# Kernel tuning notes

Hardware: AMD Instinct MI355X
Metric: run time of the kernel (lower is better)

Reference implementation:

```python
import jax, jax.numpy as jnp
import numpy as np

ALPHA = 0.2  # LeakyReLU negative slope
NEG_INF = -9e15


def setup_inputs() -> dict:
    key = jax.random.key(0)
    k1, k2, k3, k4, k5 = jax.random.split(key, 5)
    B, N, D = 4, 4096, 256
    feat = jax.random.normal(k1, (B, N, D), dtype=jnp.float32)
    adj = jax.random.randint(k2, (B, N, N), 0, 2, dtype=jnp.int32)
    W = jax.random.normal(k3, (D, D), dtype=jnp.float32) * (1.414 / np.sqrt(D))
    a_1 = jax.random.normal(k4, (D, 1), dtype=jnp.float32) * 0.1
    a_2 = jax.random.normal(k5, (D, 1), dtype=jnp.float32) * 0.1
    return {"feat": feat, "adj": adj, "W": W, "a_1": a_1, "a_2": a_2}


def reference(feat, adj, W, a_1, a_2):
    # h: [B, N, D]
    h = jnp.matmul(feat, W)
    Ax = jnp.matmul(h, a_1)  # [B, N, 1]
    Ay = jnp.matmul(h, a_2)  # [B, N, 1]
    # logits[b, i, j] = Ax[b, j] + Ay[b, i]
    logits = jnp.swapaxes(Ax, 1, 2) + Ay  # [B, N, N]
    e = jax.nn.leaky_relu(logits, negative_slope=ALPHA)
    e = jnp.where(adj > 0, e, jnp.float32(NEG_INF))
    attention = jax.nn.softmax(e, axis=-1)  # dropout p=0.0 -> identity
    h_prime = jnp.matmul(attention, feat)  # [B, N, in_features]
    h_out = jnp.matmul(h_prime, W)  # [B, N, out_features]
    return jax.nn.elu(h_out)
```

## Files before the change

kernel.cpp:

```cpp
#include <hip/hip_runtime.h>

typedef __attribute__((ext_vector_type(8))) short short8;
typedef __attribute__((ext_vector_type(4))) float f32x4;
typedef __attribute__((ext_vector_type(4))) int i32x4;
typedef __attribute__((ext_vector_type(2))) unsigned u32x2;

#define LOG2E 1.44269504f

__device__ __forceinline__ short f2bf(float f) {
  unsigned u = __builtin_bit_cast(unsigned, f);
  u += 0x7fffu + ((u >> 16) & 1u);
  return (short)(u >> 16);
}

__global__ __launch_bounds__(256) void gat_pro(
    const float* __restrict__ feat, const float* __restrict__ W,
    const float* __restrict__ a1, const float* __restrict__ a2,
    short* __restrict__ featB, short* __restrict__ WB,
    float* __restrict__ AxL, float* __restrict__ AyL) {
  __shared__ __align__(16) float a1f[256], a2f[256];
  __shared__ __align__(16) float w1f[256], w2f[256];
  __shared__ __align__(16) float tile[32][260];
  const int tid = threadIdx.x;
  const int f = blockIdx.x, b = blockIdx.y;

  a1f[tid] = a1[tid];
  a2f[tid] = a2[tid];
  __syncthreads();

  {
    float s1 = 0.f, s2 = 0.f;
    const float4* wr = (const float4*)(W + (size_t)tid * 256);
    for (int d0 = 0; d0 < 64; ++d0) {
      float4 v = wr[d0];
      s1 += v.x * a1f[d0 * 4] + v.y * a1f[d0 * 4 + 1] + v.z * a1f[d0 * 4 + 2] + v.w * a1f[d0 * 4 + 3];
      s2 += v.x * a2f[d0 * 4] + v.y * a2f[d0 * 4 + 1] + v.z * a2f[d0 * 4 + 2] + v.w * a2f[d0 * 4 + 3];
    }
    w1f[tid] = s1;
    w2f[tid] = s2;
  }
  __syncthreads();

  {
    const int r = tid >> 3, g8 = tid & 7;
    const float* frow = feat + ((size_t)(b * 4096 + f * 32 + r)) * 256;
    float s1 = 0.f, s2 = 0.f;
#pragma unroll
    for (int k = 0; k < 8; ++k) {
      const int c4 = g8 + 8 * k;
      float4 v = *(const float4*)(frow + c4 * 4);
      float4 u1 = *(const float4*)&w1f[c4 * 4];
      float4 u2 = *(const float4*)&w2f[c4 * 4];
      s1 += v.x * u1.x + v.y * u1.y + v.z * u1.z + v.w * u1.w;
      s2 += v.x * u2.x + v.y * u2.y + v.z * u2.z + v.w * u2.w;
      *(float4*)&tile[r][c4 * 4] = v;
    }
#pragma unroll
    for (int off = 4; off >= 1; off >>= 1) {
      s1 += __shfl_xor(s1, off);
      s2 += __shfl_xor(s2, off);
    }
    if (g8 == 0) {
      AxL[b * 4096 + f * 32 + r] = s1 * LOG2E;
      AyL[b * 4096 + f * 32 + r] = s2 * LOG2E;
    }
  }
  __syncthreads();

  {
    const int g = tid >> 4, l15 = tid & 15;
    short* d = featB + (((size_t)((b * 128 + f) * 16 + g)) * 64) * 8;
#pragma unroll
    for (int q = 0; q < 4; ++q) {
      short8 v;
#pragma unroll
      for (int j8 = 0; j8 < 8; ++j8) v[j8] = f2bf(tile[q * 8 + j8][g * 16 + l15]);
      *(short8*)(d + (q * 16 + l15) * 8) = v;
    }
  }

  if (b == 0 && f < 8) {
    const int g = tid >> 4, l15 = tid & 15;
    const float* s = W + ((size_t)f * 32) * 256 + g * 16 + l15;
    short* d = WB + (((size_t)(f * 16 + g)) * 64) * 8;
#pragma unroll
    for (int q = 0; q < 4; ++q) {
      short8 v;
#pragma unroll
      for (int j8 = 0; j8 < 8; ++j8) v[j8] = f2bf(s[(q * 8 + j8) * 256]);
      *(short8*)(d + (q * 16 + l15) * 8) = v;
    }
  }
}

__global__ __launch_bounds__(512, 2) void gat_attn(
    const short* __restrict__ featB,
    const int* __restrict__ adj,
    const float* __restrict__ AxL, const float* __restrict__ AyL,
    const short* __restrict__ WB,
    float* __restrict__ out)
{
  __shared__ short smem[33792];
  __shared__ float mred[8];

  const int tid = threadIdx.x;
  const int blk = blockIdx.x;
  const int x = blk & 7;
  const int b = x >> 1;
  const int it = ((blk >> 3) << 1) | (x & 1);
  const int i0 = it << 6;
  const int scoff = (blk >> 3) & 15;

  const int lane = tid & 63;
  const int aw = tid >> 6;

  const float* axb = AxL + b * 4096;
  float mx = -3.4e38f;
  for (int i = tid; i < 4096; i += 512) mx = fmaxf(mx, axb[i]);
#pragma unroll
  for (int off = 32; off >= 1; off >>= 1) mx = fmaxf(mx, __shfl_xor(mx, off));
  if (lane == 0) mred[aw] = mx;
  __syncthreads();
  const float MbLb = fmaxf(fmaxf(fmaxf(mred[0], mred[1]), fmaxf(mred[2], mred[3])),
                           fmaxf(fmaxf(mred[4], mred[5]), fmaxf(mred[6], mred[7])));

  float aLk[8], ddk[8];
#pragma unroll
  for (int k = 0; k < 8; ++k) {
    float ayL = AyL[b * 4096 + i0 + aw * 8 + k];
    float sL = ayL + MbLb;
    float mrL = fmaxf(sL, 0.2f * sL);
    aLk[k] = ayL - mrL;
    ddk[k] = -0.8f * mrL;
  }
  const int* adjr = adj + ((size_t)(b * 4096 + i0 + aw * 8)) * 4096 + lane * 4;
  const float4* axp = (const float4*)(AxL + b * 4096) + lane;

  const int cg2 = aw << 1;
  const int l15 = lane & 15;
  const int q = lane >> 4;

  f32x4 acc[4][2], lac[4];
#pragma unroll
  for (int r = 0; r < 4; ++r) {
    lac[r] = (f32x4){0.f, 0.f, 0.f, 0.f};
#pragma unroll
    for (int j = 0; j < 2; ++j) acc[r][j] = (f32x4){0.f, 0.f, 0.f, 0.f};
  }

  short8 ones;
#pragma unroll
  for (int j = 0; j < 8; ++j) ones[j] = (short)0x3F80;

  const short* fbb = featB + (size_t)b * 128 * 16 * 64 * 8 + lane * 8;

  i32x4 adv[8];
  float4 axv;
  {
    const int w0 = scoff;
    axv = axp[w0 * 64];
#pragma unroll
    for (int k = 0; k < 8; ++k)
      adv[k] = __builtin_nontemporal_load((const i32x4*)(adjr) + (size_t)k * 1024 + w0 * 64);
  }

  for (int sc = 0; sc < 16; ++sc) {
    const int wsc = (scoff + sc) & 15;
    const int pb = (sc & 1) * 16896;
    {
      const float* af = (const float*)&axv;
#pragma unroll
      for (int k = 0; k < 8; ++k) {
        unsigned pr[4];
#pragma unroll
        for (int u = 0; u < 4; ++u) {
          float v = af[u] + aLk[k];
          float uu = fmaxf(v, fmaf(0.2f, v, ddk[k]));
          unsigned ub = adv[k][u] > 0 ? __builtin_bit_cast(unsigned, uu) : 0xFF800000u;
          float p = __builtin_amdgcn_exp2f(__builtin_bit_cast(float, ub));
          pr[u] = __builtin_bit_cast(unsigned, p) + 0x8000u;
        }
        u32x2 pw;
        pw[0] = __builtin_amdgcn_perm(pr[1], pr[0], 0x07060302u);
        pw[1] = __builtin_amdgcn_perm(pr[3], pr[2], 0x07060302u);
        *(u32x2*)(smem + pb + (aw * 8 + k) * 264 + lane * 4) = pw;
      }
    }
    __syncthreads();

    if (sc < 15) {
      const int wn = (scoff + sc + 1) & 15;
      axv = axp[wn * 64];
#pragma unroll
      for (int k = 0; k < 8; ++k)
        adv[k] = __builtin_nontemporal_load((const i32x4*)(adjr) + (size_t)k * 1024 + wn * 64);
    }

#pragma unroll
    for (int h = 0; h < 8; ++h) {
      const int f = wsc * 8 + h;
      const short* fb = fbb + (((size_t)f * 16 + cg2) << 9);
      short8 a[4];
#pragma unroll
      for (int r = 0; r < 4; ++r)
        a[r] = *(const short8*)(smem + pb + (r * 16 + l15) * 264 + h * 32 + q * 8);
#pragma unroll
      for (int r = 0; r < 4; ++r)
        lac[r] = __builtin_amdgcn_mfma_f32_16x16x32_bf16(a[r], ones, lac[r], 0, 0, 0);
#pragma unroll
      for (int ct = 0; ct < 2; ++ct) {
        short8 bf = *(const short8*)(fb + (ct << 9));
#pragma unroll
        for (int r = 0; r < 4; ++r)
          acc[r][ct] = __builtin_amdgcn_mfma_f32_16x16x32_bf16(a[r], bf, acc[r][ct], 0, 0, 0);
      }
    }
  }

  float linv[4][4];
#pragma unroll
  for (int r = 0; r < 4; ++r)
#pragma unroll
    for (int reg = 0; reg < 4; ++reg) {
      float l = lac[r][reg];
      linv[r][reg] = l > 0.f ? 1.f / l : 0.f;
    }

  __syncthreads();
  short* hbuf = smem;
#pragma unroll
  for (int r = 0; r < 4; ++r)
#pragma unroll
    for (int reg = 0; reg < 4; ++reg) {
      const int lr = r * 16 + q * 4 + reg;
#pragma unroll
      for (int ct = 0; ct < 2; ++ct)
        hbuf[lr * 264 + (cg2 + ct) * 16 + l15] = f2bf(acc[r][ct][reg] * linv[r][reg]);
    }
  __syncthreads();

  const int rowg = (aw & 1) << 4;
  const int cgrp = (aw >> 1) << 2;

  f32x4 ac2[2][4];
#pragma unroll
  for (int r = 0; r < 2; ++r)
#pragma unroll
    for (int j = 0; j < 4; ++j) ac2[r][j] = (f32x4){0.f, 0.f, 0.f, 0.f};

  const short* wbb = WB + lane * 8;
#pragma unroll
  for (int f = 0; f < 8; ++f) {
    short8 a0 = *(const short8*)&hbuf[(rowg + l15) * 264 + f * 32 + q * 8];
    short8 a1 = *(const short8*)&hbuf[(rowg + 32 + l15) * 264 + f * 32 + q * 8];
    const short* wb = wbb + (((size_t)f * 16 + cgrp) << 9);
#pragma unroll
    for (int ct = 0; ct < 4; ++ct) {
      short8 bf = *(const short8*)(wb + (ct << 9));
      ac2[0][ct] = __builtin_amdgcn_mfma_f32_16x16x32_bf16(a0, bf, ac2[0][ct], 0, 0, 0);
      ac2[1][ct] = __builtin_amdgcn_mfma_f32_16x16x32_bf16(a1, bf, ac2[1][ct], 0, 0, 0);
    }
  }

#pragma unroll
  for (int r = 0; r < 2; ++r)
#pragma unroll
    for (int reg = 0; reg < 4; ++reg) {
      const int row = i0 + rowg + r * 32 + q * 4 + reg;
      float* orow = out + ((size_t)(b * 4096 + row)) * 256 + cgrp * 16 + l15;
#pragma unroll
      for (int ct = 0; ct < 4; ++ct) {
        float v = ac2[r][ct][reg];
        float o = v > 0.f ? v : (__builtin_amdgcn_exp2f(v * LOG2E) - 1.f);
        __builtin_nontemporal_store(o, orow + ct * 16);
      }
    }
}

extern "C" void kernel_launch(void* const* d_in, const int* in_sizes, int n_in,
                              void* d_out, int out_size, void* d_ws, size_t ws_size,
                              hipStream_t stream) {
  (void)in_sizes; (void)n_in; (void)out_size; (void)ws_size;
  const float* feat = (const float*)d_in[0];
  const int* adj = (const int*)d_in[1];
  const float* W = (const float*)d_in[2];
  const float* a1 = (const float*)d_in[3];
  const float* a2 = (const float*)d_in[4];
  float* out = (float*)d_out;

  char* ws = (char*)d_ws;
  short* featB   = (short*)ws;
  short* WB      = (short*)(ws + 8388608);
  float* AxL     = (float*)(ws + 8519680);
  float* AyL     = (float*)(ws + 8585216);

  hipLaunchKernelGGL(gat_pro, dim3(128, 4), dim3(256), 0, stream, feat, W, a1, a2, featB, WB, AxL, AyL);
  hipLaunchKernelGGL(gat_attn, dim3(256), dim3(512), 0, stream, featB, adj, AxL, AyL, WB, out);
}
```

Baseline: 410.0 us.

## Prefetch adjacency two super-chunks ahead with ping-pong register buffers

Restructures the main loop into unrolled even/odd pairs, each with its own register buffer for adjacency and Ax values. The global loads for a chunk are now issued two iterations ahead instead of one, giving them more time to cover memory latency. __syncthreads is replaced by an explicit LDS waitcnt plus s_barrier, so the barrier no longer waits on outstanding global loads. The cost is a second set of prefetch registers, which may lower occupancy or cause spills.

```diff
diff --git a/kernel.cpp b/kernel.cpp
--- a/kernel.cpp
+++ b/kernel.cpp
@@ -154,48 +154,33 @@
 
   const short* fbb = featB + (size_t)b * 128 * 16 * 64 * 8 + lane * 8;
 
-  i32x4 adv[8];
-  float4 axv;
-  {
-    const int w0 = scoff;
-    axv = axp[w0 * 64];
-#pragma unroll
-    for (int k = 0; k < 8; ++k)
-      adv[k] = __builtin_nontemporal_load((const i32x4*)(adjr) + (size_t)k * 1024 + w0 * 64);
-  }
-
-  for (int sc = 0; sc < 16; ++sc) {
+  i32x4 advE[8], advO[8];
+  float4 axvE, axvO;
+
+  auto phase1 = [&](int sc, const i32x4 (&advU)[8], const float4& axvU) {
+    const int pb = (sc & 1) * 16896;
+    const float* af = (const float*)&axvU;
+#pragma unroll
+    for (int k = 0; k < 8; ++k) {
+      unsigned pr[4];
+#pragma unroll
+      for (int u = 0; u < 4; ++u) {
+        float v = af[u] + aLk[k];
+        float uu = fmaxf(v, fmaf(0.2f, v, ddk[k]));
+        unsigned ub = advU[k][u] > 0 ? __builtin_bit_cast(unsigned, uu) : 0xFF800000u;
+        float p = __builtin_amdgcn_exp2f(__builtin_bit_cast(float, ub));
+        pr[u] = __builtin_bit_cast(unsigned, p) + 0x8000u;
+      }
+      u32x2 pw;
+      pw[0] = __builtin_amdgcn_perm(pr[1], pr[0], 0x07060302u);
+      pw[1] = __builtin_amdgcn_perm(pr[3], pr[2], 0x07060302u);
+      *(u32x2*)(smem + pb + (aw * 8 + k) * 264 + lane * 4) = pw;
+    }
+  };
+
+  auto phase2 = [&](int sc) {
     const int wsc = (scoff + sc) & 15;
     const int pb = (sc & 1) * 16896;
-    {
-      const float* af = (const float*)&axv;
-#pragma unroll
-      for (int k = 0; k < 8; ++k) {
-        unsigned pr[4];
-#pragma unroll
-        for (int u = 0; u < 4; ++u) {
-          float v = af[u] + aLk[k];
-          float uu = fmaxf(v, fmaf(0.2f, v, ddk[k]));
-          unsigned ub = adv[k][u] > 0 ? __builtin_bit_cast(unsigned, uu) : 0xFF800000u;
-          float p = __builtin_amdgcn_exp2f(__builtin_bit_cast(float, ub));
-          pr[u] = __builtin_bit_cast(unsigned, p) + 0x8000u;
-        }
-        u32x2 pw;
-        pw[0] = __builtin_amdgcn_perm(pr[1], pr[0], 0x07060302u);
-        pw[1] = __builtin_amdgcn_perm(pr[3], pr[2], 0x07060302u);
-        *(u32x2*)(smem + pb + (aw * 8 + k) * 264 + lane * 4) = pw;
-      }
-    }
-    __syncthreads();
-
-    if (sc < 15) {
-      const int wn = (scoff + sc + 1) & 15;
-      axv = axp[wn * 64];
-#pragma unroll
-      for (int k = 0; k < 8; ++k)
-        adv[k] = __builtin_nontemporal_load((const i32x4*)(adjr) + (size_t)k * 1024 + wn * 64);
-    }
-
 #pragma unroll
     for (int h = 0; h < 8; ++h) {
       const int f = wsc * 8 + h;
@@ -214,6 +199,49 @@
         for (int r = 0; r < 4; ++r)
           acc[r][ct] = __builtin_amdgcn_mfma_f32_16x16x32_bf16(a[r], bf, acc[r][ct], 0, 0, 0);
       }
+    }
+  };
+
+  {
+    const int w0 = scoff, w1 = (scoff + 1) & 15;
+    axvE = axp[w0 * 64];
+#pragma unroll
+    for (int k = 0; k < 8; ++k)
+      advE[k] = __builtin_nontemporal_load((const i32x4*)(adjr) + (size_t)k * 1024 + w0 * 64);
+    axvO = axp[w1 * 64];
+#pragma unroll
+    for (int k = 0; k < 8; ++k)
+      advO[k] = __builtin_nontemporal_load((const i32x4*)(adjr) + (size_t)k * 1024 + w1 * 64);
+  }
+
+  for (int scp = 0; scp < 8; ++scp) {
+    {
+      const int sc = 2 * scp;
+      phase1(sc, advE, axvE);
+      asm volatile("s_waitcnt lgkmcnt(0)" ::: "memory");
+      __builtin_amdgcn_s_barrier();
+      if (sc < 14) {
+        const int wn = (scoff + sc + 2) & 15;
+        axvE = axp[wn * 64];
+#pragma unroll
+        for (int k = 0; k < 8; ++k)
+          advE[k] = __builtin_nontemporal_load((const i32x4*)(adjr) + (size_t)k * 1024 + wn * 64);
+      }
+      phase2(sc);
+    }
+    {
+      const int sc = 2 * scp + 1;
+      phase1(sc, advO, axvO);
+      asm volatile("s_waitcnt lgkmcnt(0)" ::: "memory");
+      __builtin_amdgcn_s_barrier();
+      if (sc < 14) {
+        const int wn = (scoff + sc + 2) & 15;
+        axvO = axp[wn * 64];
+#pragma unroll
+        for (int k = 0; k < 8; ++k)
+          advO[k] = __builtin_nontemporal_load((const i32x4*)(adjr) + (size_t)k * 1024 + wn * 64);
+      }
+      phase2(sc);
     }
   }
 
```

Measured after the change: 409.7 us. About the same (-0.1%).

## Double chunk width per pipeline stage with dynamic shared memory and fewer barriers

Applied to the files above, without the earlier changes.

The column chunk per pipeline step grows from 256 to 512 columns, so the loop runs 8 iterations instead of 16. Each iteration prefetches twice as many adjacency vectors, and the double-buffered probability tile moves to about 130KB of dynamic shared memory. The goal is to halve the number of block barriers and give each step more MFMA work to hide global loads behind. The costs are occupancy dropping to one block per CU (launch bounds 512,1) and more registers held for prefetched adjacency data.

```diff
diff --git a/kernel.cpp b/kernel.cpp
--- a/kernel.cpp
+++ b/kernel.cpp
@@ -93,14 +93,14 @@
   }
 }
 
-__global__ __launch_bounds__(512, 2) void gat_attn(
+extern "C" __global__ __launch_bounds__(512, 1) void gat_attn(
     const short* __restrict__ featB,
     const int* __restrict__ adj,
     const float* __restrict__ AxL, const float* __restrict__ AyL,
     const short* __restrict__ WB,
     float* __restrict__ out)
 {
-  __shared__ short smem[33792];
+  extern __shared__ short smem[];
   __shared__ float mred[8];
 
   const int tid = threadIdx.x;
@@ -109,7 +109,7 @@
   const int b = x >> 1;
   const int it = ((blk >> 3) << 1) | (x & 1);
   const int i0 = it << 6;
-  const int scoff = (blk >> 3) & 15;
+  const int scoff = (blk >> 3) & 7;
 
   const int lane = tid & 63;
   const int aw = tid >> 6;
@@ -154,56 +154,68 @@
 
   const short* fbb = featB + (size_t)b * 128 * 16 * 64 * 8 + lane * 8;
 
-  i32x4 adv[8];
-  float4 axv;
+  i32x4 adv[16];
+  float4 axv0, axv1;
+
   {
-    const int w0 = scoff;
-    axv = axp[w0 * 64];
-#pragma unroll
-    for (int k = 0; k < 8; ++k)
-      adv[k] = __builtin_nontemporal_load((const i32x4*)(adjr) + (size_t)k * 1024 + w0 * 64);
-  }
-
-  for (int sc = 0; sc < 16; ++sc) {
-    const int wsc = (scoff + sc) & 15;
-    const int pb = (sc & 1) * 16896;
+    const int w = scoff;
+    axv0 = axp[w * 128];
+    axv1 = axp[w * 128 + 64];
+#pragma unroll
+    for (int k = 0; k < 8; ++k) {
+      adv[k * 2 + 0] = __builtin_nontemporal_load((const i32x4*)(adjr) + (size_t)k * 1024 + w * 128);
+      adv[k * 2 + 1] = __builtin_nontemporal_load((const i32x4*)(adjr) + (size_t)k * 1024 + w * 128 + 64);
+    }
+  }
+
+  for (int sc = 0; sc < 8; ++sc) {
+    const int wsc = (scoff + sc) & 7;
+    const int pb = (sc & 1) * 33280;
     {
-      const float* af = (const float*)&axv;
 #pragma unroll
       for (int k = 0; k < 8; ++k) {
-        unsigned pr[4];
-#pragma unroll
-        for (int u = 0; u < 4; ++u) {
-          float v = af[u] + aLk[k];
-          float uu = fmaxf(v, fmaf(0.2f, v, ddk[k]));
-          unsigned ub = adv[k][u] > 0 ? __builtin_bit_cast(unsigned, uu) : 0xFF800000u;
-          float p = __builtin_amdgcn_exp2f(__builtin_bit_cast(float, ub));
-          pr[u] = __builtin_bit_cast(unsigned, p) + 0x8000u;
+#pragma unroll
+        for (int c = 0; c < 2; ++c) {
+          const float* af = (c == 0) ? (const float*)&axv0 : (const float*)&axv1;
+          const i32x4 ad = adv[k * 2 + c];
+          unsigned pr[4];
+#pragma unroll
+          for (int u = 0; u < 4; ++u) {
+            float v = af[u] + aLk[k];
+            float uu = fmaxf(v, fmaf(0.2f, v, ddk[k]));
+            unsigned ub = ad[u] > 0 ? __builtin_bit_cast(unsigned, uu) : 0xFF800000u;
+            float p = __builtin_amdgcn_exp2f(__builtin_bit_cast(float, ub));
+            pr[u] = __builtin_bit_cast(unsigned, p) + 0x8000u;
+          }
+          u32x2 pw;
+          pw[0] = __builtin_amdgcn_perm(pr[1], pr[0], 0x07060302u);
+          pw[1] = __builtin_amdgcn_perm(pr[3], pr[2], 0x07060302u);
+          *(u32x2*)(smem + pb + (aw * 8 + k) * 520 + c * 256 + lane * 4) = pw;
         }
-        u32x2 pw;
-        pw[0] = __builtin_amdgcn_perm(pr[1], pr[0], 0x07060302u);
-        pw[1] = __builtin_amdgcn_perm(pr[3], pr[2], 0x07060302u);
-        *(u32x2*)(smem + pb + (aw * 8 + k) * 264 + lane * 4) = pw;
       }
     }
-    __syncthreads();
-
-    if (sc < 15) {
-      const int wn = (scoff + sc + 1) & 15;
-      axv = axp[wn * 64];
-#pragma unroll
-      for (int k = 0; k < 8; ++k)
-        adv[k] = __builtin_nontemporal_load((const i32x4*)(adjr) + (size_t)k * 1024 + wn * 64);
-    }
-
-#pragma unroll
-    for (int h = 0; h < 8; ++h) {
-      const int f = wsc * 8 + h;
+    asm volatile("s_waitcnt lgkmcnt(0)" ::: "memory");
+    __builtin_amdgcn_s_barrier();
+
+    if (sc < 7) {
+      const int wn = (scoff + sc + 1) & 7;
+      axv0 = axp[wn * 128];
+      axv1 = axp[wn * 128 + 64];
+#pragma unroll
+      for (int k = 0; k < 8; ++k) {
+        adv[k * 2 + 0] = __builtin_nontemporal_load((const i32x4*)(adjr) + (size_t)k * 1024 + wn * 128);
+        adv[k * 2 + 1] = __builtin_nontemporal_load((const i32x4*)(adjr) + (size_t)k * 1024 + wn * 128 + 64);
+      }
+    }
+
+#pragma unroll
+    for (int h = 0; h < 16; ++h) {
+      const int f = wsc * 16 + h;
       const short* fb = fbb + (((size_t)f * 16 + cg2) << 9);
       short8 a[4];
 #pragma unroll
       for (int r = 0; r < 4; ++r)
-        a[r] = *(const short8*)(smem + pb + (r * 16 + l15) * 264 + h * 32 + q * 8);
+        a[r] = *(const short8*)(smem + pb + (r * 16 + l15) * 520 + h * 32 + q * 8);
 #pragma unroll
       for (int r = 0; r < 4; ++r)
         lac[r] = __builtin_amdgcn_mfma_f32_16x16x32_bf16(a[r], ones, lac[r], 0, 0, 0);
@@ -295,5 +307,5 @@
   float* AyL     = (float*)(ws + 8585216);
 
   hipLaunchKernelGGL(gat_pro, dim3(128, 4), dim3(256), 0, stream, feat, W, a1, a2, featB, WB, AxL, AyL);
-  hipLaunchKernelGGL(gat_attn, dim3(256), dim3(512), 0, stream, featB, adj, AxL, AyL, WB, out);
+  hipLaunchKernelGGL(gat_attn, dim3(256), dim3(512), 133120, stream, featB, adj, AxL, AyL, WB, out);
 }
```

New measurement: 423.5 us. 1.03x slower.

## Use 1024-thread blocks in attention kernel, halving per-wave rows and columns

Applied to the files above, without the earlier changes.

Doubles the attention kernel's block size to 16 waves. Each wave now handles 4 adjacency rows and one 16-column output group instead of 8 rows and two groups, so per-thread registers drop and more waves are resident to hide adjacency-load latency. The __syncthreads in the main loop becomes an explicit lgkmcnt wait plus s_barrier, which no longer waits for the in-flight prefetch loads. The risk is that the per-sc barrier now spans 16 waves, and launch_bounds(1024,4) may not be attainable with 66KB of shared memory per block, which could limit occupancy.

```diff
diff --git a/kernel.cpp b/kernel.cpp
--- a/kernel.cpp
+++ b/kernel.cpp
@@ -93,7 +93,7 @@
   }
 }
 
-__global__ __launch_bounds__(512, 2) void gat_attn(
+__global__ __launch_bounds__(1024, 4) void gat_attn(
     const short* __restrict__ featB,
     const int* __restrict__ adj,
     const float* __restrict__ AxL, const float* __restrict__ AyL,
@@ -101,7 +101,7 @@
     float* __restrict__ out)
 {
   __shared__ short smem[33792];
-  __shared__ float mred[8];
+  __shared__ float mred[16];
 
   const int tid = threadIdx.x;
   const int blk = blockIdx.x;
@@ -113,39 +113,37 @@
 
   const int lane = tid & 63;
   const int aw = tid >> 6;
+  const int l15 = lane & 15;
+  const int q = lane >> 4;
 
   const float* axb = AxL + b * 4096;
   float mx = -3.4e38f;
-  for (int i = tid; i < 4096; i += 512) mx = fmaxf(mx, axb[i]);
+  for (int i = tid; i < 4096; i += 1024) mx = fmaxf(mx, axb[i]);
 #pragma unroll
   for (int off = 32; off >= 1; off >>= 1) mx = fmaxf(mx, __shfl_xor(mx, off));
   if (lane == 0) mred[aw] = mx;
   __syncthreads();
-  const float MbLb = fmaxf(fmaxf(fmaxf(mred[0], mred[1]), fmaxf(mred[2], mred[3])),
-                           fmaxf(fmaxf(mred[4], mred[5]), fmaxf(mred[6], mred[7])));
-
-  float aLk[8], ddk[8];
-#pragma unroll
-  for (int k = 0; k < 8; ++k) {
-    float ayL = AyL[b * 4096 + i0 + aw * 8 + k];
+  float MbLb = mred[0];
+#pragma unroll
+  for (int i = 1; i < 16; ++i) MbLb = fmaxf(MbLb, mred[i]);
+
+  float aLk[4], ddk[4];
+#pragma unroll
+  for (int k = 0; k < 4; ++k) {
+    float ayL = AyL[b * 4096 + i0 + aw * 4 + k];
     float sL = ayL + MbLb;
     float mrL = fmaxf(sL, 0.2f * sL);
     aLk[k] = ayL - mrL;
     ddk[k] = -0.8f * mrL;
   }
-  const int* adjr = adj + ((size_t)(b * 4096 + i0 + aw * 8)) * 4096 + lane * 4;
+  const int* adjr = adj + ((size_t)(b * 4096 + i0 + aw * 4)) * 4096 + lane * 4;
   const float4* axp = (const float4*)(AxL + b * 4096) + lane;
 
-  const int cg2 = aw << 1;
-  const int l15 = lane & 15;
-  const int q = lane >> 4;
-
-  f32x4 acc[4][2], lac[4];
+  f32x4 acc[4], lac[4];
 #pragma unroll
   for (int r = 0; r < 4; ++r) {
     lac[r] = (f32x4){0.f, 0.f, 0.f, 0.f};
-#pragma unroll
-    for (int j = 0; j < 2; ++j) acc[r][j] = (f32x4){0.f, 0.f, 0.f, 0.f};
+    acc[r] = (f32x4){0.f, 0.f, 0.f, 0.f};
   }
 
   short8 ones;
@@ -154,14 +152,13 @@
 
   const short* fbb = featB + (size_t)b * 128 * 16 * 64 * 8 + lane * 8;
 
-  i32x4 adv[8];
+  i32x4 adv[4];
   float4 axv;
   {
-    const int w0 = scoff;
-    axv = axp[w0 * 64];
-#pragma unroll
-    for (int k = 0; k < 8; ++k)
-      adv[k] = __builtin_nontemporal_load((const i32x4*)(adjr) + (size_t)k * 1024 + w0 * 64);
+    axv = axp[scoff * 64];
+#pragma unroll
+    for (int k = 0; k < 4; ++k)
+      adv[k] = __builtin_nontemporal_load((const i32x4*)(adjr) + (size_t)k * 1024 + scoff * 64);
   }
 
   for (int sc = 0; sc < 16; ++sc) {
@@ -170,7 +167,7 @@
     {
       const float* af = (const float*)&axv;
 #pragma unroll
-      for (int k = 0; k < 8; ++k) {
+      for (int k = 0; k < 4; ++k) {
         unsigned pr[4];
 #pragma unroll
         for (int u = 0; u < 4; ++u) {
@@ -183,23 +180,24 @@
         u32x2 pw;
         pw[0] = __builtin_amdgcn_perm(pr[1], pr[0], 0x07060302u);
         pw[1] = __builtin_amdgcn_perm(pr[3], pr[2], 0x07060302u);
-        *(u32x2*)(smem + pb + (aw * 8 + k) * 264 + lane * 4) = pw;
+        *(u32x2*)(smem + pb + (aw * 4 + k) * 264 + lane * 4) = pw;
       }
     }
-    __syncthreads();
+    asm volatile("s_waitcnt lgkmcnt(0)" ::: "memory");
+    __builtin_amdgcn_s_barrier();
 
     if (sc < 15) {
       const int wn = (scoff + sc + 1) & 15;
       axv = axp[wn * 64];
 #pragma unroll
-      for (int k = 0; k < 8; ++k)
+      for (int k = 0; k < 4; ++k)
         adv[k] = __builtin_nontemporal_load((const i32x4*)(adjr) + (size_t)k * 1024 + wn * 64);
     }
 
 #pragma unroll
     for (int h = 0; h < 8; ++h) {
       const int f = wsc * 8 + h;
-      const short* fb = fbb + (((size_t)f * 16 + cg2) << 9);
+      const short* fb = fbb + (((size_t)f * 16 + aw) << 9);
       short8 a[4];
 #pragma unroll
       for (int r = 0; r < 4; ++r)
@@ -207,13 +205,10 @@
 #pragma unroll
       for (int r = 0; r < 4; ++r)
         lac[r] = __builtin_amdgcn_mfma_f32_16x16x32_bf16(a[r], ones, lac[r], 0, 0, 0);
-#pragma unroll
-      for (int ct = 0; ct < 2; ++ct) {
-        short8 bf = *(const short8*)(fb + (ct << 9));
-#pragma unroll
-        for (int r = 0; r < 4; ++r)
-          acc[r][ct] = __builtin_amdgcn_mfma_f32_16x16x32_bf16(a[r], bf, acc[r][ct], 0, 0, 0);
-      }
+      short8 bf = *(const short8*)fb;
+#pragma unroll
+      for (int r = 0; r < 4; ++r)
+        acc[r] = __builtin_amdgcn_mfma_f32_16x16x32_bf16(a[r], bf, acc[r], 0, 0, 0);
     }
   }
 
@@ -233,48 +228,40 @@
 #pragma unroll
     for (int reg = 0; reg < 4; ++reg) {
       const int lr = r * 16 + q * 4 + reg;
-#pragma unroll
-      for (int ct = 0; ct < 2; ++ct)
-        hbuf[lr * 264 + (cg2 + ct) * 16 + l15] = f2bf(acc[r][ct][reg] * linv[r][reg]);
-    }
-  __syncthreads();
-
-  const int rowg = (aw & 1) << 4;
-  const int cgrp = (aw >> 1) << 2;
-
-  f32x4 ac2[2][4];
-#pragma unroll
-  for (int r = 0; r < 2; ++r)
-#pragma unroll
-    for (int j = 0; j < 4; ++j) ac2[r][j] = (f32x4){0.f, 0.f, 0.f, 0.f};
+      hbuf[lr * 264 + aw * 16 + l15] = f2bf(acc[r][reg] * linv[r][reg]);
+    }
+  __syncthreads();
+
+  const int rowg16 = (aw & 3) << 4;
+  const int cgrp = (aw >> 2) << 2;
+
+  f32x4 ac2[4];
+#pragma unroll
+  for (int j = 0; j < 4; ++j) ac2[j] = (f32x4){0.f, 0.f, 0.f, 0.f};
 
   const short* wbb = WB + lane * 8;
 #pragma unroll
   for (int f = 0; f < 8; ++f) {
-    short8 a0 = *(const short8*)&hbuf[(rowg + l15) * 264 + f * 32 + q * 8];
-    short8 a1 = *(const short8*)&hbuf[(rowg + 32 + l15) * 264 + f * 32 + q * 8];
+    short8 a0 = *(const short8*)&hbuf[(rowg16 + l15) * 264 + f * 32 + q * 8];
     const short* wb = wbb + (((size_t)f * 16 + cgrp) << 9);
 #pragma unroll
     for (int ct = 0; ct < 4; ++ct) {
       short8 bf = *(const short8*)(wb + (ct << 9));
-      ac2[0][ct] = __builtin_amdgcn_mfma_f32_16x16x32_bf16(a0, bf, ac2[0][ct], 0, 0, 0);
-      ac2[1][ct] = __builtin_amdgcn_mfma_f32_16x16x32_bf16(a1, bf, ac2[1][ct], 0, 0, 0);
-    }
-  }
-
-#pragma unroll
-  for (int r = 0; r < 2; ++r)
-#pragma unroll
-    for (int reg = 0; reg < 4; ++reg) {
-      const int row = i0 + rowg + r * 32 + q * 4 + reg;
-      float* orow = out + ((size_t)(b * 4096 + row)) * 256 + cgrp * 16 + l15;
-#pragma unroll
-      for (int ct = 0; ct < 4; ++ct) {
-        float v = ac2[r][ct][reg];
-        float o = v > 0.f ? v : (__builtin_amdgcn_exp2f(v * LOG2E) - 1.f);
-        __builtin_nontemporal_store(o, orow + ct * 16);
-      }
-    }
+      ac2[ct] = __builtin_amdgcn_mfma_f32_16x16x32_bf16(a0, bf, ac2[ct], 0, 0, 0);
+    }
+  }
+
+#pragma unroll
+  for (int reg = 0; reg < 4; ++reg) {
+    const int row = i0 + rowg16 + q * 4 + reg;
+    float* orow = out + ((size_t)(b * 4096 + row)) * 256 + cgrp * 16 + l15;
+#pragma unroll
+    for (int ct = 0; ct < 4; ++ct) {
+      float v = ac2[ct][reg];
+      float o = v > 0.f ? v : (__builtin_amdgcn_exp2f(v * LOG2E) - 1.f);
+      __builtin_nontemporal_store(o, orow + ct * 16);
+    }
+  }
 }
 
 extern "C" void kernel_launch(void* const* d_in, const int* in_sizes, int n_in,
@@ -295,5 +282,5 @@
   float* AyL     = (float*)(ws + 8585216);
 
   hipLaunchKernelGGL(gat_pro, dim3(128, 4), dim3(256), 0, stream, feat, W, a1, a2, featB, WB, AxL, AyL);
-  hipLaunchKernelGGL(gat_attn, dim3(256), dim3(512), 0, stream, featB, adj, AxL, AyL, WB, out);
-}
+  hipLaunchKernelGGL(gat_attn, dim3(256), dim3(1024), 0, stream, featB, adj, AxL, AyL, WB, out);
+}
```

Measured after the change: 411.9 us. About the same (+0.4%).
